# Kernel optimization log

Measured on AMD Instinct MI355X. Metric: run time of the kernel, lower is better.

The kernel has to match this reference:

```python
import jax, jax.numpy as jnp
import numpy as np

N = 50000   # nodes
E = 800000  # edges
D = 64      # hidden_channels (= in_channels)
L = 3       # num_layers
G = 512     # graphs in batch
S = 32      # s_channels
BN_EPS = 1e-5


def setup_inputs() -> dict:
    key = jax.random.key(0)
    ks = jax.random.split(key, 10)
    x = jax.random.normal(ks[0], (N, D), dtype=jnp.float32)
    edge_index = jax.random.randint(ks[1], (2, E), 0, N)
    batch = jnp.sort(jax.random.randint(ks[2], (N,), 0, G))
    mapping = jax.random.randint(ks[3], (G,), 0, N)
    edge_weight = jax.random.uniform(ks[4], (E,), dtype=jnp.float32)
    pooling_mask = jnp.ones((N,), dtype=jnp.float32)
    # per-layer GIN MLP params (stacked over layers)
    W1 = 0.05 * jax.random.normal(ks[5], (L, D, D), dtype=jnp.float32)
    b1 = jnp.zeros((L, D), jnp.float32)
    gamma = jnp.ones((L, D), jnp.float32)
    beta = jnp.zeros((L, D), jnp.float32)
    bn_mean = jnp.zeros((L, D), jnp.float32)
    bn_var = jnp.ones((L, D), jnp.float32)
    W2 = 0.05 * jax.random.normal(ks[6], (L, D, D), dtype=jnp.float32)
    b2 = jnp.zeros((L, D), jnp.float32)
    eps = jnp.zeros((L,), jnp.float32)  # train_eps=True, init 0
    lin_w = 0.05 * jax.random.normal(ks[7], (2 * D * L, S), dtype=jnp.float32)
    lin_b = jnp.zeros((S,), jnp.float32)
    return dict(x=x, edge_weight=edge_weight, pooling_mask=pooling_mask,
                W1=W1, b1=b1, gamma=gamma, beta=beta, bn_mean=bn_mean,
                bn_var=bn_var, W2=W2, b2=b2, eps=eps, lin_w=lin_w,
                lin_b=lin_b, edge_index=edge_index, batch=batch,
                mapping=mapping)


def _sgin_forward(x, edge_weight, pooling_mask, W1, b1, gamma, beta,
                  bn_mean, bn_var, W2, b2, eps, lin_w, lin_b,
                  edge_index, batch, mapping):
    src, dst = edge_index[0], edge_index[1]
    h = x  # dropout is identity in eval mode
    pooled = []
    for i in range(L):
        # GIN aggregation: sum_j w_ij * h_j  at target nodes
        msg = h[src] * edge_weight[:, None]            # [E, D]
        agg = jax.ops.segment_sum(msg, dst, num_segments=N)
        z = (1.0 + eps[i]) * h + agg                   # [N, D]
        # MLP: Linear -> BN(eval) -> ReLU -> Linear -> ReLU
        z = z @ W1[i] + b1[i]
        z = gamma[i] * (z - bn_mean[i]) * jax.lax.rsqrt(bn_var[i] + BN_EPS) + beta[i]
        z = jax.nn.relu(z)
        h = jax.nn.relu(z @ W2[i] + b2[i])
        # per-layer pooling: masked global add pool || center-node gather
        emb_add = jax.ops.segment_sum(h * pooling_mask[:, None], batch,
                                      num_segments=G)  # [G, D]
        emb_center = h[mapping]                          # [G, D]
        pooled.append(jnp.concatenate([emb_add, emb_center], axis=-1))
    hcat = jnp.concatenate(pooled, axis=1)               # [G, 2*D*L]
    return hcat @ lin_w + lin_b                          # [G, S]


def reference(x, edge_weight, pooling_mask, W1, b1, gamma, beta, bn_mean,
              bn_var, W2, b2, eps, lin_w, lin_b, edge_index, batch, mapping):
    return _sgin_forward(x, edge_weight, pooling_mask, W1, b1, gamma, beta,
                         bn_mean, bn_var, W2, b2, eps, lin_w, lin_b,
                         edge_index, batch, mapping)
```

## Files before the change

kernel.cpp:

```cpp
#include <hip/hip_runtime.h>
#include <hip/hip_fp16.h>

#define DD 64
#define HC 384
#define SS 32
#define BINW 256
#define BSH 8
#define CAP 8192
#define CHUNK 4096

__global__ __launch_bounds__(256) void prep_kernel(
    const float* __restrict__ x, __half* __restrict__ hh0,
    int* __restrict__ bin_cur, float* __restrict__ hcat,
    int nbins, int hcat4, int total)
{
  int gid = blockIdx.x * 256 + threadIdx.x;
  if (gid < nbins) bin_cur[gid] = gid * CAP;
  if (gid < hcat4) ((float4*)hcat)[gid] = make_float4(0.f, 0.f, 0.f, 0.f);
  int i = gid * 8;
  if (i < total) {
    float4 a = *(const float4*)(x + i);
    float4 b = *(const float4*)(x + i + 4);
    __half2 o[4];
    o[0] = __floats2half2_rn(a.x, a.y);
    o[1] = __floats2half2_rn(a.z, a.w);
    o[2] = __floats2half2_rn(b.x, b.y);
    o[3] = __floats2half2_rn(b.z, b.w);
    *(float4*)(hh0 + i) = *(float4*)o;
  }
}

__global__ __launch_bounds__(256) void bin_part_kernel(
    const int* __restrict__ ei, const float* __restrict__ ew,
    int* __restrict__ bin_cur, unsigned* __restrict__ pk_slab,
    unsigned short* __restrict__ dl_slab, int E)
{
  __shared__ unsigned spk[CHUNK];
  __shared__ unsigned short sdst[CHUNK];
  __shared__ int bcnt[256], boff[256], bcur[256], gbase[256], stmp[256];
  int t = threadIdx.x;
  int e0 = blockIdx.x * CHUNK;
  int m = min(CHUNK, E - e0);
  bcnt[t] = 0;
  __syncthreads();
  for (int i = t; i < m; i += 256)
    atomicAdd(&bcnt[ei[E + e0 + i] >> BSH], 1);
  __syncthreads();
  int v = bcnt[t];
  stmp[t] = v;
  __syncthreads();
  for (int o = 1; o < 256; o <<= 1) {
    int u = (t >= o) ? stmp[t - o] : 0;
    __syncthreads();
    stmp[t] += u;
    __syncthreads();
  }
  boff[t] = stmp[t] - v;
  bcur[t] = stmp[t] - v;
  if (v > 0) gbase[t] = atomicAdd(&bin_cur[t], v);
  __syncthreads();
  for (int i = t; i < m; i += 256) {
    unsigned d = (unsigned)ei[E + e0 + i];
    int b = d >> BSH;
    int p = atomicAdd(&bcur[b], 1);
    unsigned short wh = __half_as_ushort(__float2half(ew[e0 + i]));
    spk[p] = (unsigned)ei[e0 + i] | ((unsigned)wh << 16);
    sdst[p] = (unsigned short)d;
  }
  __syncthreads();
  for (int i = t; i < m; i += 256) {
    unsigned short d = sdst[i];
    int b = d >> BSH;
    int g = gbase[b] + (i - boff[b]);
    pk_slab[g] = spk[i];
    dl_slab[g] = d;
  }
}

__global__ __launch_bounds__(256) void fine_csr_kernel(
    const unsigned* __restrict__ pk_slab,
    const unsigned short* __restrict__ dl_slab,
    const int* __restrict__ bin_cur, int* __restrict__ beg,
    int* __restrict__ endo, unsigned* __restrict__ packed, int N)
{
  __shared__ int cnt[256], loff[256], cur[256], stmp[256];
  int t = threadIdx.x;
  int b = blockIdx.x;
  int sbase = b * CAP;
  int m = bin_cur[b] - sbase;
  cnt[t] = 0;
  __syncthreads();
  for (int i = t; i < m; i += 256)
    atomicAdd(&cnt[dl_slab[sbase + i] & 255], 1);
  __syncthreads();
  int v = cnt[t];
  stmp[t] = v;
  __syncthreads();
  for (int o = 1; o < 256; o <<= 1) {
    int u = (t >= o) ? stmp[t - o] : 0;
    __syncthreads();
    stmp[t] += u;
    __syncthreads();
  }
  loff[t] = stmp[t] - v;
  cur[t] = loff[t];
  int node = b * BINW + t;
  if (node < N) {
    beg[node] = sbase + loff[t];
    endo[node] = sbase + loff[t] + v;
  }
  __syncthreads();
  for (int i = t; i < m; i += 256) {
    int dl = dl_slab[sbase + i] & 255;
    int p = atomicAdd(&cur[dl], 1);
    packed[sbase + p] = pk_slab[sbase + i];
  }
}

__global__ __launch_bounds__(256) void gather_kernel(
    const __half* __restrict__ hh, const unsigned* __restrict__ packed,
    const int* __restrict__ begA, const int* __restrict__ endA,
    const float* __restrict__ epsv, float* __restrict__ z, int layer, int N)
{
  int wave = threadIdx.x >> 6;
  int lane = threadIdx.x & 63;
  int sub = lane >> 3;
  int ch0 = (lane & 7) * 8;
  int n = blockIdx.x * 4 + wave;
  if (n >= N) return;
  int beg = begA[n], end = endA[n];
  float acc[8] = {0, 0, 0, 0, 0, 0, 0, 0};
  int e = beg + sub;
  for (; e + 8 < end; e += 16) {
    unsigned p0 = packed[e];
    unsigned p1 = packed[e + 8];
    float4 r0 = *(const float4*)(hh + (size_t)(p0 & 0xffffu) * DD + ch0);
    float4 r1 = *(const float4*)(hh + (size_t)(p1 & 0xffffu) * DD + ch0);
    float w0 = __half2float(__ushort_as_half((unsigned short)(p0 >> 16)));
    float w1 = __half2float(__ushort_as_half((unsigned short)(p1 >> 16)));
    const __half2* H0 = (const __half2*)&r0;
    const __half2* H1 = (const __half2*)&r1;
    #pragma unroll
    for (int j = 0; j < 4; ++j) {
      float2 f0 = __half22float2(H0[j]);
      float2 f1 = __half22float2(H1[j]);
      acc[2 * j]     = fmaf(w0, f0.x, acc[2 * j]);
      acc[2 * j + 1] = fmaf(w0, f0.y, acc[2 * j + 1]);
      acc[2 * j]     = fmaf(w1, f1.x, acc[2 * j]);
      acc[2 * j + 1] = fmaf(w1, f1.y, acc[2 * j + 1]);
    }
  }
  for (; e < end; e += 8) {
    unsigned p = packed[e];
    float4 rr = *(const float4*)(hh + (size_t)(p & 0xffffu) * DD + ch0);
    float w = __half2float(__ushort_as_half((unsigned short)(p >> 16)));
    const __half2* H = (const __half2*)&rr;
    #pragma unroll
    for (int j = 0; j < 4; ++j) {
      float2 f = __half22float2(H[j]);
      acc[2 * j]     = fmaf(w, f.x, acc[2 * j]);
      acc[2 * j + 1] = fmaf(w, f.y, acc[2 * j + 1]);
    }
  }
  #pragma unroll
  for (int j = 0; j < 8; ++j) {
    acc[j] += __shfl_xor(acc[j], 8);
    acc[j] += __shfl_xor(acc[j], 16);
    acc[j] += __shfl_xor(acc[j], 32);
  }
  if (sub == 0) {
    float e1 = 1.0f + epsv[layer];
    float4 sr = *(const float4*)(hh + (size_t)n * DD + ch0);
    const __half2* S = (const __half2*)&sr;
    float4 o0, o1;
    float2 s0 = __half22float2(S[0]), s1 = __half22float2(S[1]);
    float2 s2 = __half22float2(S[2]), s3 = __half22float2(S[3]);
    o0.x = fmaf(e1, s0.x, acc[0]); o0.y = fmaf(e1, s0.y, acc[1]);
    o0.z = fmaf(e1, s1.x, acc[2]); o0.w = fmaf(e1, s1.y, acc[3]);
    o1.x = fmaf(e1, s2.x, acc[4]); o1.y = fmaf(e1, s2.y, acc[5]);
    o1.z = fmaf(e1, s3.x, acc[6]); o1.w = fmaf(e1, s3.y, acc[7]);
    *(float4*)(z + (size_t)n * DD + ch0) = o0;
    *(float4*)(z + (size_t)n * DD + ch0 + 4) = o1;
  }
}

__global__ __launch_bounds__(256) void node_kernel(
    const float* __restrict__ z, __half* __restrict__ hhout,
    const float* __restrict__ W1, const float* __restrict__ b1,
    const float* __restrict__ gamma, const float* __restrict__ beta,
    const float* __restrict__ bnm, const float* __restrict__ bnv,
    const float* __restrict__ W2, const float* __restrict__ b2,
    const float* __restrict__ pmask, const int* __restrict__ batch,
    float* __restrict__ hcat, int layer, int N)
{
  __shared__ float tileZ[DD * DD];
  __shared__ float tileT[DD * DD];
  const int wave = threadIdx.x >> 6;
  const int lane = threadIdx.x & 63;
  const int n0 = blockIdx.x * 64;
  const int c0 = __builtin_amdgcn_readfirstlane(wave * 16);
  const float* W1l = W1 + layer * DD * DD;
  const float* W2l = W2 + layer * DD * DD;

  #pragma unroll
  for (int i = 0; i < 16; ++i) {
    int r = c0 + i;
    int n = n0 + r;
    float v = (n < N) ? z[(size_t)n * DD + lane] : 0.0f;
    tileZ[r * DD + ((lane + r) & 63)] = v;
  }
  __syncthreads();

  float t[16];
  #pragma unroll
  for (int cc = 0; cc < 16; ++cc) t[cc] = 0.0f;
  #pragma unroll 2
  for (int k = 0; k < DD; ++k) {
    float zk = tileZ[lane * DD + ((k + lane) & 63)];
    #pragma unroll
    for (int cc = 0; cc < 16; ++cc)
      t[cc] = fmaf(zk, W1l[k * DD + c0 + cc], t[cc]);
  }
  #pragma unroll
  for (int cc = 0; cc < 16; ++cc) {
    int c = c0 + cc;
    float A = gamma[layer * DD + c] * rsqrtf(bnv[layer * DD + c] + 1e-5f);
    float B = fmaf(b1[layer * DD + c] - bnm[layer * DD + c], A,
                   beta[layer * DD + c]);
    tileT[lane * DD + ((c + lane) & 63)] = fmaxf(fmaf(t[cc], A, B), 0.0f);
  }
  __syncthreads();

  #pragma unroll
  for (int cc = 0; cc < 16; ++cc) t[cc] = 0.0f;
  #pragma unroll 2
  for (int k = 0; k < DD; ++k) {
    float zk = tileT[lane * DD + ((k + lane) & 63)];
    #pragma unroll
    for (int cc = 0; cc < 16; ++cc)
      t[cc] = fmaf(zk, W2l[k * DD + c0 + cc], t[cc]);
  }
  #pragma unroll
  for (int cc = 0; cc < 16; ++cc) {
    int c = c0 + cc;
    tileZ[lane * DD + ((c + lane) & 63)] =
        fmaxf(t[cc] + b2[layer * DD + c], 0.0f);
  }
  __syncthreads();

  float accp = 0.0f;
  int gcur = -1;
  for (int i = 0; i < 16; ++i) {
    int r = c0 + i;
    int n = n0 + r;
    if (n >= N) break;
    float v = tileZ[r * DD + ((lane + r) & 63)];
    hhout[(size_t)n * DD + lane] = __float2half(v);
    int g = batch[n];
    if (g != gcur) {
      if (gcur >= 0) atomicAdd(&hcat[gcur * HC + layer * 128 + lane], accp);
      gcur = g; accp = 0.0f;
    }
    accp = fmaf(v, pmask[n], accp);
  }
  if (gcur >= 0) atomicAdd(&hcat[gcur * HC + layer * 128 + lane], accp);
}

__global__ __launch_bounds__(256) void final_kernel(
    const float* __restrict__ hcat, const __half* __restrict__ h1,
    const __half* __restrict__ h2, const __half* __restrict__ h3,
    const int* __restrict__ mapping, const float* __restrict__ lw,
    const float* __restrict__ lb, float* __restrict__ out, int G)
{
  int gid = blockIdx.x * 256 + threadIdx.x;
  int g = gid >> 5, s = gid & 31;
  if (g >= G) return;
  float acc = lb[s];
  size_t mrow = (size_t)mapping[g] * DD;
  #pragma unroll
  for (int l = 0; l < 3; ++l) {
    const float* hc = hcat + g * HC + l * 128;
    const float* lwa = lw + (l * 128) * SS + s;
    #pragma unroll 4
    for (int c = 0; c < 64; ++c)
      acc = fmaf(hc[c], lwa[c * SS], acc);
    const __half* hr = ((l == 0) ? h1 : ((l == 1) ? h2 : h3)) + mrow;
    const float* lwc = lw + (l * 128 + 64) * SS + s;
    #pragma unroll 4
    for (int c = 0; c < 64; ++c)
      acc = fmaf(__half2float(hr[c]), lwc[c * SS], acc);
  }
  out[g * SS + s] = acc;
}

extern "C" void kernel_launch(void* const* d_in, const int* in_sizes, int n_in,
                              void* d_out, int out_size, void* d_ws, size_t ws_size,
                              hipStream_t stream)
{
  const float* x     = (const float*)d_in[0];
  const float* ew    = (const float*)d_in[1];
  const float* pmask = (const float*)d_in[2];
  const float* W1    = (const float*)d_in[3];
  const float* b1    = (const float*)d_in[4];
  const float* gma   = (const float*)d_in[5];
  const float* bta   = (const float*)d_in[6];
  const float* bnm   = (const float*)d_in[7];
  const float* bnv   = (const float*)d_in[8];
  const float* W2    = (const float*)d_in[9];
  const float* b2    = (const float*)d_in[10];
  const float* epsv  = (const float*)d_in[11];
  const float* lw    = (const float*)d_in[12];
  const float* lb    = (const float*)d_in[13];
  const int*   ei    = (const int*)d_in[14];
  const int*   batch = (const int*)d_in[15];
  const int*   mapping = (const int*)d_in[16];

  const int N = in_sizes[2];
  const int E = in_sizes[1];
  const int G = in_sizes[16];
  const int nbins = (N + BINW - 1) / BINW;
  const int nchunks = (E + CHUNK - 1) / CHUNK;

  __half*   hh0  = (__half*)d_ws;
  __half*   hh1  = hh0 + (size_t)N * DD;
  __half*   hh2  = hh1 + (size_t)N * DD;
  __half*   hh3  = hh2 + (size_t)N * DD;
  float*    zscr = (float*)(hh3 + (size_t)N * DD);
  float*    hcat = zscr + (size_t)N * DD;
  int*      beg  = (int*)(hcat + (size_t)G * HC);
  int*      endo = beg + N;
  int*      bin_cur = endo + N;
  unsigned* packed  = (unsigned*)(bin_cur + 256);
  unsigned* pk_slab = packed + (size_t)nbins * CAP;
  unsigned short* dl_slab =
      (unsigned short*)(pk_slab + (size_t)nbins * CAP);
  float* fout = (float*)d_out;

  prep_kernel<<<(N * DD / 8 + 255) / 256, 256, 0, stream>>>(
      x, hh0, bin_cur, hcat, nbins, G * HC / 4, N * DD);

  bin_part_kernel<<<nchunks, 256, 0, stream>>>(ei, ew, bin_cur,
                                               pk_slab, dl_slab, E);
  fine_csr_kernel<<<nbins, 256, 0, stream>>>(pk_slab, dl_slab, bin_cur,
                                             beg, endo, packed, N);

  __half* hhs[4] = {hh0, hh1, hh2, hh3};
  for (int layer = 0; layer < 3; ++layer) {
    gather_kernel<<<(N + 3) / 4, 256, 0, stream>>>(
        hhs[layer], packed, beg, endo, epsv, zscr, layer, N);
    node_kernel<<<(N + 63) / 64, 256, 0, stream>>>(
        zscr, hhs[layer + 1], W1, b1, gma, bta, bnm, bnv, W2, b2,
        pmask, batch, hcat, layer, N);
  }
  final_kernel<<<(G * SS + 255) / 256, 256, 0, stream>>>(
      hcat, hh1, hh2, hh3, mapping, lw, lb, fout, G);
}
```

Before: 314.1 us.

## Fuse per-layer gather, MLP and final kernels into one cooperative persistent kernel

Replaces the seven per-layer gather/node launches and the final projection launch with a single cooperative persistent kernel. Grid-wide syncs separate the aggregation, MLP and pooling phases, and the kernel loops over layers internally. This removes kernel launch gaps and tail effects between the small kernels. The costs are grid.sync overhead, a grid capped by occupancy (launch_bounds 256,6), and sharing one LDS tile instead of two, which adds extra __syncthreads.

```diff
diff --git a/kernel.cpp b/kernel.cpp
--- a/kernel.cpp
+++ b/kernel.cpp
@@ -1,5 +1,8 @@
 #include <hip/hip_runtime.h>
 #include <hip/hip_fp16.h>
+#include <hip/hip_cooperative_groups.h>
+
+namespace cg = cooperative_groups;
 
 #define DD 64
 #define HC 384
@@ -117,180 +120,188 @@
   }
 }
 
-__global__ __launch_bounds__(256) void gather_kernel(
-    const __half* __restrict__ hh, const unsigned* __restrict__ packed,
-    const int* __restrict__ begA, const int* __restrict__ endA,
-    const float* __restrict__ epsv, float* __restrict__ z, int layer, int N)
-{
-  int wave = threadIdx.x >> 6;
-  int lane = threadIdx.x & 63;
-  int sub = lane >> 3;
-  int ch0 = (lane & 7) * 8;
-  int n = blockIdx.x * 4 + wave;
-  if (n >= N) return;
-  int beg = begA[n], end = endA[n];
-  float acc[8] = {0, 0, 0, 0, 0, 0, 0, 0};
-  int e = beg + sub;
-  for (; e + 8 < end; e += 16) {
-    unsigned p0 = packed[e];
-    unsigned p1 = packed[e + 8];
-    float4 r0 = *(const float4*)(hh + (size_t)(p0 & 0xffffu) * DD + ch0);
-    float4 r1 = *(const float4*)(hh + (size_t)(p1 & 0xffffu) * DD + ch0);
-    float w0 = __half2float(__ushort_as_half((unsigned short)(p0 >> 16)));
-    float w1 = __half2float(__ushort_as_half((unsigned short)(p1 >> 16)));
-    const __half2* H0 = (const __half2*)&r0;
-    const __half2* H1 = (const __half2*)&r1;
-    #pragma unroll
-    for (int j = 0; j < 4; ++j) {
-      float2 f0 = __half22float2(H0[j]);
-      float2 f1 = __half22float2(H1[j]);
-      acc[2 * j]     = fmaf(w0, f0.x, acc[2 * j]);
-      acc[2 * j + 1] = fmaf(w0, f0.y, acc[2 * j + 1]);
-      acc[2 * j]     = fmaf(w1, f1.x, acc[2 * j]);
-      acc[2 * j + 1] = fmaf(w1, f1.y, acc[2 * j + 1]);
-    }
-  }
-  for (; e < end; e += 8) {
-    unsigned p = packed[e];
-    float4 rr = *(const float4*)(hh + (size_t)(p & 0xffffu) * DD + ch0);
-    float w = __half2float(__ushort_as_half((unsigned short)(p >> 16)));
-    const __half2* H = (const __half2*)&rr;
-    #pragma unroll
-    for (int j = 0; j < 4; ++j) {
-      float2 f = __half22float2(H[j]);
-      acc[2 * j]     = fmaf(w, f.x, acc[2 * j]);
-      acc[2 * j + 1] = fmaf(w, f.y, acc[2 * j + 1]);
-    }
-  }
-  #pragma unroll
-  for (int j = 0; j < 8; ++j) {
-    acc[j] += __shfl_xor(acc[j], 8);
-    acc[j] += __shfl_xor(acc[j], 16);
-    acc[j] += __shfl_xor(acc[j], 32);
-  }
-  if (sub == 0) {
-    float e1 = 1.0f + epsv[layer];
-    float4 sr = *(const float4*)(hh + (size_t)n * DD + ch0);
-    const __half2* S = (const __half2*)&sr;
-    float4 o0, o1;
-    float2 s0 = __half22float2(S[0]), s1 = __half22float2(S[1]);
-    float2 s2 = __half22float2(S[2]), s3 = __half22float2(S[3]);
-    o0.x = fmaf(e1, s0.x, acc[0]); o0.y = fmaf(e1, s0.y, acc[1]);
-    o0.z = fmaf(e1, s1.x, acc[2]); o0.w = fmaf(e1, s1.y, acc[3]);
-    o1.x = fmaf(e1, s2.x, acc[4]); o1.y = fmaf(e1, s2.y, acc[5]);
-    o1.z = fmaf(e1, s3.x, acc[6]); o1.w = fmaf(e1, s3.y, acc[7]);
-    *(float4*)(z + (size_t)n * DD + ch0) = o0;
-    *(float4*)(z + (size_t)n * DD + ch0 + 4) = o1;
-  }
-}
-
-__global__ __launch_bounds__(256) void node_kernel(
-    const float* __restrict__ z, __half* __restrict__ hhout,
+__global__ __launch_bounds__(256, 6) void mega_kernel(
+    const __half* __restrict__ hh0, __half* __restrict__ hh1,
+    __half* __restrict__ hh2, __half* __restrict__ hh3,
+    const unsigned* __restrict__ packed, const int* __restrict__ begA,
+    const int* __restrict__ endA, const float* __restrict__ epsv,
+    float* __restrict__ zscr,
     const float* __restrict__ W1, const float* __restrict__ b1,
     const float* __restrict__ gamma, const float* __restrict__ beta,
     const float* __restrict__ bnm, const float* __restrict__ bnv,
     const float* __restrict__ W2, const float* __restrict__ b2,
     const float* __restrict__ pmask, const int* __restrict__ batch,
-    float* __restrict__ hcat, int layer, int N)
-{
+    float* __restrict__ hcat, const int* __restrict__ mapping,
+    const float* __restrict__ lw, const float* __restrict__ lb,
+    float* __restrict__ out, int N, int G)
+{
+  cg::grid_group grid = cg::this_grid();
   __shared__ float tileZ[DD * DD];
-  __shared__ float tileT[DD * DD];
   const int wave = threadIdx.x >> 6;
   const int lane = threadIdx.x & 63;
-  const int n0 = blockIdx.x * 64;
+  const int sub = lane >> 3;
+  const int ch0 = (lane & 7) * 8;
   const int c0 = __builtin_amdgcn_readfirstlane(wave * 16);
-  const float* W1l = W1 + layer * DD * DD;
-  const float* W2l = W2 + layer * DD * DD;
-
-  #pragma unroll
-  for (int i = 0; i < 16; ++i) {
-    int r = c0 + i;
-    int n = n0 + r;
-    float v = (n < N) ? z[(size_t)n * DD + lane] : 0.0f;
-    tileZ[r * DD + ((lane + r) & 63)] = v;
-  }
-  __syncthreads();
-
-  float t[16];
-  #pragma unroll
-  for (int cc = 0; cc < 16; ++cc) t[cc] = 0.0f;
-  #pragma unroll 2
-  for (int k = 0; k < DD; ++k) {
-    float zk = tileZ[lane * DD + ((k + lane) & 63)];
+  const int nquads = (N + 3) / 4;
+  const int ntiles = (N + 63) / 64;
+
+  for (int layer = 0; layer < 3; ++layer) {
+    const __half* hh = (layer == 0) ? hh0 : (layer == 1) ? hh1 : hh2;
+    __half* hho = (layer == 0) ? hh1 : (layer == 1) ? hh2 : hh3;
+    const float e1 = 1.0f + epsv[layer];
+    const float* W1l = W1 + layer * DD * DD;
+    const float* W2l = W2 + layer * DD * DD;
+
+    for (int q = blockIdx.x; q < nquads; q += gridDim.x) {
+      int n = q * 4 + wave;
+      if (n < N) {
+        int beg = begA[n], end = endA[n];
+        float acc[8] = {0, 0, 0, 0, 0, 0, 0, 0};
+        int e = beg + sub;
+        for (; e + 8 < end; e += 16) {
+          unsigned p0 = packed[e];
+          unsigned p1 = packed[e + 8];
+          float4 r0 = *(const float4*)(hh + (size_t)(p0 & 0xffffu) * DD + ch0);
+          float4 r1 = *(const float4*)(hh + (size_t)(p1 & 0xffffu) * DD + ch0);
+          float w0 = __half2float(__ushort_as_half((unsigned short)(p0 >> 16)));
+          float w1 = __half2float(__ushort_as_half((unsigned short)(p1 >> 16)));
+          const __half2* H0 = (const __half2*)&r0;
+          const __half2* H1 = (const __half2*)&r1;
+          #pragma unroll
+          for (int j = 0; j < 4; ++j) {
+            float2 f0 = __half22float2(H0[j]);
+            float2 f1 = __half22float2(H1[j]);
+            acc[2 * j]     = fmaf(w0, f0.x, acc[2 * j]);
+            acc[2 * j + 1] = fmaf(w0, f0.y, acc[2 * j + 1]);
+            acc[2 * j]     = fmaf(w1, f1.x, acc[2 * j]);
+            acc[2 * j + 1] = fmaf(w1, f1.y, acc[2 * j + 1]);
+          }
+        }
+        for (; e < end; e += 8) {
+          unsigned p = packed[e];
+          float4 rr = *(const float4*)(hh + (size_t)(p & 0xffffu) * DD + ch0);
+          float w = __half2float(__ushort_as_half((unsigned short)(p >> 16)));
+          const __half2* H = (const __half2*)&rr;
+          #pragma unroll
+          for (int j = 0; j < 4; ++j) {
+            float2 f = __half22float2(H[j]);
+            acc[2 * j]     = fmaf(w, f.x, acc[2 * j]);
+            acc[2 * j + 1] = fmaf(w, f.y, acc[2 * j + 1]);
+          }
+        }
+        #pragma unroll
+        for (int j = 0; j < 8; ++j) {
+          acc[j] += __shfl_xor(acc[j], 8);
+          acc[j] += __shfl_xor(acc[j], 16);
+          acc[j] += __shfl_xor(acc[j], 32);
+        }
+        if (sub == 0) {
+          float4 sr = *(const float4*)(hh + (size_t)n * DD + ch0);
+          const __half2* S = (const __half2*)&sr;
+          float2 s0 = __half22float2(S[0]), s1 = __half22float2(S[1]);
+          float2 s2 = __half22float2(S[2]), s3 = __half22float2(S[3]);
+          float4 o0, o1;
+          o0.x = fmaf(e1, s0.x, acc[0]); o0.y = fmaf(e1, s0.y, acc[1]);
+          o0.z = fmaf(e1, s1.x, acc[2]); o0.w = fmaf(e1, s1.y, acc[3]);
+          o1.x = fmaf(e1, s2.x, acc[4]); o1.y = fmaf(e1, s2.y, acc[5]);
+          o1.z = fmaf(e1, s3.x, acc[6]); o1.w = fmaf(e1, s3.y, acc[7]);
+          *(float4*)(zscr + (size_t)n * DD + ch0) = o0;
+          *(float4*)(zscr + (size_t)n * DD + ch0 + 4) = o1;
+        }
+      }
+    }
+    grid.sync();
+
+    for (int tile = blockIdx.x; tile < ntiles; tile += gridDim.x) {
+      int n0 = tile * 64;
+      #pragma unroll
+      for (int i = 0; i < 16; ++i) {
+        int r = c0 + i;
+        int n = n0 + r;
+        float v = (n < N) ? zscr[(size_t)n * DD + lane] : 0.0f;
+        tileZ[r * DD + ((lane + r) & 63)] = v;
+      }
+      __syncthreads();
+      float t[16];
+      #pragma unroll
+      for (int cc = 0; cc < 16; ++cc) t[cc] = 0.0f;
+      #pragma unroll 2
+      for (int k = 0; k < DD; ++k) {
+        float zk = tileZ[lane * DD + ((k + lane) & 63)];
+        #pragma unroll
+        for (int cc = 0; cc < 16; ++cc)
+          t[cc] = fmaf(zk, W1l[k * DD + c0 + cc], t[cc]);
+      }
+      __syncthreads();
+      #pragma unroll
+      for (int cc = 0; cc < 16; ++cc) {
+        int c = c0 + cc;
+        float A = gamma[layer * DD + c] * rsqrtf(bnv[layer * DD + c] + 1e-5f);
+        float B = fmaf(b1[layer * DD + c] - bnm[layer * DD + c], A,
+                       beta[layer * DD + c]);
+        tileZ[lane * DD + ((c + lane) & 63)] = fmaxf(fmaf(t[cc], A, B), 0.0f);
+      }
+      __syncthreads();
+      #pragma unroll
+      for (int cc = 0; cc < 16; ++cc) t[cc] = 0.0f;
+      #pragma unroll 2
+      for (int k = 0; k < DD; ++k) {
+        float zk = tileZ[lane * DD + ((k + lane) & 63)];
+        #pragma unroll
+        for (int cc = 0; cc < 16; ++cc)
+          t[cc] = fmaf(zk, W2l[k * DD + c0 + cc], t[cc]);
+      }
+      __syncthreads();
+      #pragma unroll
+      for (int cc = 0; cc < 16; ++cc) {
+        int c = c0 + cc;
+        tileZ[lane * DD + ((c + lane) & 63)] =
+            fmaxf(t[cc] + b2[layer * DD + c], 0.0f);
+      }
+      __syncthreads();
+      float accp = 0.0f;
+      int gcur = -1;
+      for (int i = 0; i < 16; ++i) {
+        int r = c0 + i;
+        int n = n0 + r;
+        if (n >= N) break;
+        float v = tileZ[r * DD + ((lane + r) & 63)];
+        hho[(size_t)n * DD + lane] = __float2half(v);
+        int g = batch[n];
+        if (g != gcur) {
+          if (gcur >= 0) atomicAdd(&hcat[gcur * HC + layer * 128 + lane], accp);
+          gcur = g; accp = 0.0f;
+        }
+        accp = fmaf(v, pmask[n], accp);
+      }
+      if (gcur >= 0) atomicAdd(&hcat[gcur * HC + layer * 128 + lane], accp);
+      __syncthreads();
+    }
+    grid.sync();
+  }
+
+  int nf = (G * SS + 255) / 256;
+  for (int f = blockIdx.x; f < nf; f += gridDim.x) {
+    int gid = f * 256 + threadIdx.x;
+    int g = gid >> 5, s = gid & 31;
+    if (g >= G) continue;
+    float acc = lb[s];
+    size_t mrow = (size_t)mapping[g] * DD;
     #pragma unroll
-    for (int cc = 0; cc < 16; ++cc)
-      t[cc] = fmaf(zk, W1l[k * DD + c0 + cc], t[cc]);
-  }
-  #pragma unroll
-  for (int cc = 0; cc < 16; ++cc) {
-    int c = c0 + cc;
-    float A = gamma[layer * DD + c] * rsqrtf(bnv[layer * DD + c] + 1e-5f);
-    float B = fmaf(b1[layer * DD + c] - bnm[layer * DD + c], A,
-                   beta[layer * DD + c]);
-    tileT[lane * DD + ((c + lane) & 63)] = fmaxf(fmaf(t[cc], A, B), 0.0f);
-  }
-  __syncthreads();
-
-  #pragma unroll
-  for (int cc = 0; cc < 16; ++cc) t[cc] = 0.0f;
-  #pragma unroll 2
-  for (int k = 0; k < DD; ++k) {
-    float zk = tileT[lane * DD + ((k + lane) & 63)];
-    #pragma unroll
-    for (int cc = 0; cc < 16; ++cc)
-      t[cc] = fmaf(zk, W2l[k * DD + c0 + cc], t[cc]);
-  }
-  #pragma unroll
-  for (int cc = 0; cc < 16; ++cc) {
-    int c = c0 + cc;
-    tileZ[lane * DD + ((c + lane) & 63)] =
-        fmaxf(t[cc] + b2[layer * DD + c], 0.0f);
-  }
-  __syncthreads();
-
-  float accp = 0.0f;
-  int gcur = -1;
-  for (int i = 0; i < 16; ++i) {
-    int r = c0 + i;
-    int n = n0 + r;
-    if (n >= N) break;
-    float v = tileZ[r * DD + ((lane + r) & 63)];
-    hhout[(size_t)n * DD + lane] = __float2half(v);
-    int g = batch[n];
-    if (g != gcur) {
-      if (gcur >= 0) atomicAdd(&hcat[gcur * HC + layer * 128 + lane], accp);
-      gcur = g; accp = 0.0f;
+    for (int l = 0; l < 3; ++l) {
+      const float* hc = hcat + g * HC + l * 128;
+      const float* lwa = lw + (l * 128) * SS + s;
+      #pragma unroll 4
+      for (int c = 0; c < 64; ++c)
+        acc = fmaf(hc[c], lwa[c * SS], acc);
+      const __half* hr = ((l == 0) ? hh1 : ((l == 1) ? hh2 : hh3)) + mrow;
+      const float* lwc = lw + (l * 128 + 64) * SS + s;
+      #pragma unroll 4
+      for (int c = 0; c < 64; ++c)
+        acc = fmaf(__half2float(hr[c]), lwc[c * SS], acc);
     }
-    accp = fmaf(v, pmask[n], accp);
-  }
-  if (gcur >= 0) atomicAdd(&hcat[gcur * HC + layer * 128 + lane], accp);
-}
-
-__global__ __launch_bounds__(256) void final_kernel(
-    const float* __restrict__ hcat, const __half* __restrict__ h1,
-    const __half* __restrict__ h2, const __half* __restrict__ h3,
-    const int* __restrict__ mapping, const float* __restrict__ lw,
-    const float* __restrict__ lb, float* __restrict__ out, int G)
-{
-  int gid = blockIdx.x * 256 + threadIdx.x;
-  int g = gid >> 5, s = gid & 31;
-  if (g >= G) return;
-  float acc = lb[s];
-  size_t mrow = (size_t)mapping[g] * DD;
-  #pragma unroll
-  for (int l = 0; l < 3; ++l) {
-    const float* hc = hcat + g * HC + l * 128;
-    const float* lwa = lw + (l * 128) * SS + s;
-    #pragma unroll 4
-    for (int c = 0; c < 64; ++c)
-      acc = fmaf(hc[c], lwa[c * SS], acc);
-    const __half* hr = ((l == 0) ? h1 : ((l == 1) ? h2 : h3)) + mrow;
-    const float* lwc = lw + (l * 128 + 64) * SS + s;
-    #pragma unroll 4
-    for (int c = 0; c < 64; ++c)
-      acc = fmaf(__half2float(hr[c]), lwc[c * SS], acc);
-  }
-  out[g * SS + s] = acc;
+    out[g * SS + s] = acc;
+  }
 }
 
 extern "C" void kernel_launch(void* const* d_in, const int* in_sizes, int n_in,
@@ -344,14 +355,20 @@
   fine_csr_kernel<<<nbins, 256, 0, stream>>>(pk_slab, dl_slab, bin_cur,
                                              beg, endo, packed, N);
 
-  __half* hhs[4] = {hh0, hh1, hh2, hh3};
-  for (int layer = 0; layer < 3; ++layer) {
-    gather_kernel<<<(N + 3) / 4, 256, 0, stream>>>(
-        hhs[layer], packed, beg, endo, epsv, zscr, layer, N);
-    node_kernel<<<(N + 63) / 64, 256, 0, stream>>>(
-        zscr, hhs[layer + 1], W1, b1, gma, bta, bnm, bnv, W2, b2,
-        pmask, batch, hcat, layer, N);
-  }
-  final_kernel<<<(G * SS + 255) / 256, 256, 0, stream>>>(
-      hcat, hh1, hh2, hh3, mapping, lw, lb, fout, G);
-}
+  int maxB = 0;
+  hipOccupancyMaxActiveBlocksPerMultiprocessor(&maxB, mega_kernel, 256, 0);
+  if (maxB < 1) maxB = 1;
+  if (maxB > 6) maxB = 6;
+  int NB = maxB * 256;
+
+  const __half* hh0c = hh0;
+  void* kargs[] = {
+    (void*)&hh0c, (void*)&hh1, (void*)&hh2, (void*)&hh3,
+    (void*)&packed, (void*)&beg, (void*)&endo, (void*)&epsv,
+    (void*)&zscr, (void*)&W1, (void*)&b1, (void*)&gma, (void*)&bta,
+    (void*)&bnm, (void*)&bnv, (void*)&W2, (void*)&b2, (void*)&pmask,
+    (void*)&batch, (void*)&hcat, (void*)&mapping, (void*)&lw, (void*)&lb,
+    (void*)&fout, (void*)&N, (void*)&G };
+  hipLaunchCooperativeKernel(mega_kernel, dim3(NB), dim3(256),
+                             kargs, 0, stream);
+}
```

Measured after the change: 1.005 ms. 220% more time.

## Gather four nodes per wave and store aggregated features in fp16

Applied to the files above, without the earlier changes.

The gather kernel now has each wave process four destination nodes at once, interleaving their edge loads so more independent memory requests are in flight. The aggregated z buffer moves from fp32 to fp16, which halves the bytes written by gather and read by the node MLP kernel. The risk is extra rounding error on z before the MLP. Per-node degree imbalance within a wave also causes divergence, and four accumulator sets raise register use.

```diff
diff --git a/kernel.cpp b/kernel.cpp
--- a/kernel.cpp
+++ b/kernel.cpp
@@ -120,72 +120,82 @@
 __global__ __launch_bounds__(256) void gather_kernel(
     const __half* __restrict__ hh, const unsigned* __restrict__ packed,
     const int* __restrict__ begA, const int* __restrict__ endA,
-    const float* __restrict__ epsv, float* __restrict__ z, int layer, int N)
+    const float* __restrict__ epsv, __half* __restrict__ zh, int layer, int N)
 {
   int wave = threadIdx.x >> 6;
   int lane = threadIdx.x & 63;
   int sub = lane >> 3;
   int ch0 = (lane & 7) * 8;
-  int n = blockIdx.x * 4 + wave;
-  if (n >= N) return;
-  int beg = begA[n], end = endA[n];
-  float acc[8] = {0, 0, 0, 0, 0, 0, 0, 0};
-  int e = beg + sub;
-  for (; e + 8 < end; e += 16) {
-    unsigned p0 = packed[e];
-    unsigned p1 = packed[e + 8];
-    float4 r0 = *(const float4*)(hh + (size_t)(p0 & 0xffffu) * DD + ch0);
-    float4 r1 = *(const float4*)(hh + (size_t)(p1 & 0xffffu) * DD + ch0);
-    float w0 = __half2float(__ushort_as_half((unsigned short)(p0 >> 16)));
-    float w1 = __half2float(__ushort_as_half((unsigned short)(p1 >> 16)));
-    const __half2* H0 = (const __half2*)&r0;
-    const __half2* H1 = (const __half2*)&r1;
-    #pragma unroll
-    for (int j = 0; j < 4; ++j) {
-      float2 f0 = __half22float2(H0[j]);
-      float2 f1 = __half22float2(H1[j]);
-      acc[2 * j]     = fmaf(w0, f0.x, acc[2 * j]);
-      acc[2 * j + 1] = fmaf(w0, f0.y, acc[2 * j + 1]);
-      acc[2 * j]     = fmaf(w1, f1.x, acc[2 * j]);
-      acc[2 * j + 1] = fmaf(w1, f1.y, acc[2 * j + 1]);
+  int n0 = blockIdx.x * 16 + wave * 4;
+  if (n0 >= N) return;
+  int e[4], en[4];
+  #pragma unroll
+  for (int q = 0; q < 4; ++q) {
+    int n = n0 + q;
+    bool ok = n < N;
+    e[q]  = ok ? begA[n] + sub : 0;
+    en[q] = ok ? endA[n] : 0;
+  }
+  float acc[4][8] = {};
+  while (e[0] < en[0] || e[1] < en[1] || e[2] < en[2] || e[3] < en[3]) {
+    unsigned p[4];
+    float4 r[4];
+    #pragma unroll
+    for (int q = 0; q < 4; ++q)
+      if (e[q] < en[q]) p[q] = packed[e[q]];
+    #pragma unroll
+    for (int q = 0; q < 4; ++q)
+      if (e[q] < en[q])
+        r[q] = *(const float4*)(hh + (size_t)(p[q] & 0xffffu) * DD + ch0);
+    #pragma unroll
+    for (int q = 0; q < 4; ++q) {
+      if (e[q] < en[q]) {
+        float w = __half2float(__ushort_as_half((unsigned short)(p[q] >> 16)));
+        const __half2* H = (const __half2*)&r[q];
+        #pragma unroll
+        for (int j = 0; j < 4; ++j) {
+          float2 f = __half22float2(H[j]);
+          acc[q][2 * j]     = fmaf(w, f.x, acc[q][2 * j]);
+          acc[q][2 * j + 1] = fmaf(w, f.y, acc[q][2 * j + 1]);
+        }
+      }
+      e[q] += 8;
     }
   }
-  for (; e < end; e += 8) {
-    unsigned p = packed[e];
-    float4 rr = *(const float4*)(hh + (size_t)(p & 0xffffu) * DD + ch0);
-    float w = __half2float(__ushort_as_half((unsigned short)(p >> 16)));
-    const __half2* H = (const __half2*)&rr;
-    #pragma unroll
-    for (int j = 0; j < 4; ++j) {
-      float2 f = __half22float2(H[j]);
-      acc[2 * j]     = fmaf(w, f.x, acc[2 * j]);
-      acc[2 * j + 1] = fmaf(w, f.y, acc[2 * j + 1]);
+  #pragma unroll
+  for (int q = 0; q < 4; ++q)
+    #pragma unroll
+    for (int j = 0; j < 8; ++j) {
+      acc[q][j] += __shfl_xor(acc[q][j], 8);
+      acc[q][j] += __shfl_xor(acc[q][j], 16);
+      acc[q][j] += __shfl_xor(acc[q][j], 32);
     }
-  }
-  #pragma unroll
-  for (int j = 0; j < 8; ++j) {
-    acc[j] += __shfl_xor(acc[j], 8);
-    acc[j] += __shfl_xor(acc[j], 16);
-    acc[j] += __shfl_xor(acc[j], 32);
-  }
   if (sub == 0) {
     float e1 = 1.0f + epsv[layer];
-    float4 sr = *(const float4*)(hh + (size_t)n * DD + ch0);
-    const __half2* S = (const __half2*)&sr;
-    float4 o0, o1;
-    float2 s0 = __half22float2(S[0]), s1 = __half22float2(S[1]);
-    float2 s2 = __half22float2(S[2]), s3 = __half22float2(S[3]);
-    o0.x = fmaf(e1, s0.x, acc[0]); o0.y = fmaf(e1, s0.y, acc[1]);
-    o0.z = fmaf(e1, s1.x, acc[2]); o0.w = fmaf(e1, s1.y, acc[3]);
-    o1.x = fmaf(e1, s2.x, acc[4]); o1.y = fmaf(e1, s2.y, acc[5]);
-    o1.z = fmaf(e1, s3.x, acc[6]); o1.w = fmaf(e1, s3.y, acc[7]);
-    *(float4*)(z + (size_t)n * DD + ch0) = o0;
-    *(float4*)(z + (size_t)n * DD + ch0 + 4) = o1;
+    #pragma unroll
+    for (int q = 0; q < 4; ++q) {
+      int n = n0 + q;
+      if (n >= N) break;
+      float4 sr = *(const float4*)(hh + (size_t)n * DD + ch0);
+      const __half2* S = (const __half2*)&sr;
+      float2 s0 = __half22float2(S[0]), s1 = __half22float2(S[1]);
+      float2 s2 = __half22float2(S[2]), s3 = __half22float2(S[3]);
+      __half2 o[4];
+      o[0] = __floats2half2_rn(fmaf(e1, s0.x, acc[q][0]),
+                               fmaf(e1, s0.y, acc[q][1]));
+      o[1] = __floats2half2_rn(fmaf(e1, s1.x, acc[q][2]),
+                               fmaf(e1, s1.y, acc[q][3]));
+      o[2] = __floats2half2_rn(fmaf(e1, s2.x, acc[q][4]),
+                               fmaf(e1, s2.y, acc[q][5]));
+      o[3] = __floats2half2_rn(fmaf(e1, s3.x, acc[q][6]),
+                               fmaf(e1, s3.y, acc[q][7]));
+      *(float4*)(zh + (size_t)n * DD + ch0) = *(float4*)o;
+    }
   }
 }
 
 __global__ __launch_bounds__(256) void node_kernel(
-    const float* __restrict__ z, __half* __restrict__ hhout,
+    const __half* __restrict__ zh, __half* __restrict__ hhout,
     const float* __restrict__ W1, const float* __restrict__ b1,
     const float* __restrict__ gamma, const float* __restrict__ beta,
     const float* __restrict__ bnm, const float* __restrict__ bnv,
@@ -206,7 +216,7 @@
   for (int i = 0; i < 16; ++i) {
     int r = c0 + i;
     int n = n0 + r;
-    float v = (n < N) ? z[(size_t)n * DD + lane] : 0.0f;
+    float v = (n < N) ? __half2float(zh[(size_t)n * DD + lane]) : 0.0f;
     tileZ[r * DD + ((lane + r) & 63)] = v;
   }
   __syncthreads();
@@ -325,8 +335,8 @@
   __half*   hh1  = hh0 + (size_t)N * DD;
   __half*   hh2  = hh1 + (size_t)N * DD;
   __half*   hh3  = hh2 + (size_t)N * DD;
-  float*    zscr = (float*)(hh3 + (size_t)N * DD);
-  float*    hcat = zscr + (size_t)N * DD;
+  __half*   zh   = hh3 + (size_t)N * DD;
+  float*    hcat = (float*)(zh + (size_t)N * DD);
   int*      beg  = (int*)(hcat + (size_t)G * HC);
   int*      endo = beg + N;
   int*      bin_cur = endo + N;
@@ -346,10 +356,10 @@
 
   __half* hhs[4] = {hh0, hh1, hh2, hh3};
   for (int layer = 0; layer < 3; ++layer) {
-    gather_kernel<<<(N + 3) / 4, 256, 0, stream>>>(
-        hhs[layer], packed, beg, endo, epsv, zscr, layer, N);
+    gather_kernel<<<(N + 15) / 16, 256, 0, stream>>>(
+        hhs[layer], packed, beg, endo, epsv, zh, layer, N);
     node_kernel<<<(N + 63) / 64, 256, 0, stream>>>(
-        zscr, hhs[layer + 1], W1, b1, gma, bta, bnm, bnv, W2, b2,
+        zh, hhs[layer + 1], W1, b1, gma, bta, bnm, bnv, W2, b2,
         pmask, batch, hcat, layer, N);
   }
   final_kernel<<<(G * SS + 255) / 256, 256, 0, stream>>>(
```

Result: slower. 333.5 us (+6.2%).
